# Kernel optimization log

Measured on AMD Instinct MI355X. Metric: run time of the kernel, lower is better.

## Reference

```python
import jax, jax.numpy as jnp
import numpy as np

B, L, DIM, N_STATE, K_CONV = 2, 2048, 1024, 16, 4


def setup_inputs() -> dict:
    key = jax.random.key(0)
    ks = jax.random.split(key, 6)
    sc = lambda k, shape, s: jax.random.normal(k, shape, jnp.float32) * s
    return {
        "x": jax.random.normal(ks[0], (B, L, DIM), jnp.float32),
        "in_proj_w": sc(ks[1], (2 * DIM, DIM), 0.02),
        "conv_w": sc(ks[2], (DIM, 1, K_CONV), 0.1),
        "conv_b": jnp.zeros((DIM,), jnp.float32),
        "x_proj_w": sc(ks[3], (2 * N_STATE + DIM, DIM), 0.02),
        "D_param": jnp.ones((DIM,), jnp.float32),
        "out_proj_w": sc(ks[4], (DIM, DIM), 0.02),
    }


def reference(x, in_proj_w, conv_w, conv_b, x_proj_w, D_param, out_proj_w):
    b, l, d = x.shape
    n = (x_proj_w.shape[0] - d) // 2
    k = conv_w.shape[-1]
    # A buffer: -[1..n] broadcast over channels -> [d, n]
    A = -(jnp.arange(1, n + 1, dtype=x.dtype)[None, :] * jnp.ones((d, 1), x.dtype))

    xz = x @ in_proj_w.T                       # [b, l, 2d]
    x_c, z = xz[..., :d], xz[..., d:]

    # depthwise causal conv (torch pads both sides k-1 then truncates to l == left-pad k-1)
    xc = jnp.transpose(x_c, (0, 2, 1))          # [b, d, l]
    xc = jax.lax.conv_general_dilated(
        xc, conv_w, window_strides=(1,), padding=[(k - 1, 0)],
        dimension_numbers=("NCH", "OIH", "NCH"), feature_group_count=d)
    xc = xc + conv_b[None, :, None]
    xc = jax.nn.silu(jnp.transpose(xc, (0, 2, 1)))  # [b, l, d]

    x_dbl = xc @ x_proj_w.T                    # [b, l, 2n + d]
    B_ssm = x_dbl[..., :n]                     # [b, l, n]
    C_ssm = x_dbl[..., n:2 * n]                # [b, l, n]
    dt = jax.nn.softplus(x_dbl[..., 2 * n:])   # [b, l, d]

    dA = jnp.exp(dt[..., None] * A[None, None])            # [b, l, d, n]
    dBx = (dt[..., None] * B_ssm[:, :, None, :]) * xc[..., None]  # dB * x, [b, l, d, n]

    def step(h, inputs):
        dA_t, dBx_t, C_t = inputs              # [b,d,n], [b,d,n], [b,n]
        h = h * dA_t + dBx_t
        y_t = jnp.einsum("bdn,bn->bd", h, C_t)
        return h, y_t

    h0 = jnp.zeros((b, d, n), x.dtype)
    _, ys = jax.lax.scan(
        step, h0,
        (jnp.moveaxis(dA, 1, 0), jnp.moveaxis(dBx, 1, 0), jnp.moveaxis(C_ssm, 1, 0)))
    y = jnp.moveaxis(ys, 0, 1) + D_param * xc  # [b, l, d]
    y = y * jax.nn.silu(z)
    return y @ out_proj_w.T
```

## Files before the change

kernel.cpp:

```cpp
#include <hip/hip_runtime.h>
#include <cmath>

#define BB   2
#define LL   2048
#define DIMD 1024
#define NS   16
#define KC   4
#define ML   (BB*LL)
#define XZ_N (2*DIMD)
#define XD_N (2*NS + DIMD)
#define LC   16
#define NC   (LL/LC)

typedef __attribute__((ext_vector_type(8))) short bf16x8;
typedef __attribute__((ext_vector_type(4))) float f32x4;

__device__ __forceinline__ unsigned short f2bf(float f) {
    union { float f; unsigned u; } v; v.f = f;
    unsigned r = v.u + 0x7FFF + ((v.u >> 16) & 1);
    return (unsigned short)(r >> 16);
}
__device__ __forceinline__ float bf2f(unsigned short u) {
    union { unsigned u; float f; } v; v.u = (unsigned)u << 16;
    return v.f;
}
__device__ __forceinline__ float silu_f(float a) {
    return a / (1.f + __expf(-a));
}
__device__ __forceinline__ void dt_decay(float raw, float& dt, float& e) {
    const float t = __expf(fminf(raw, 80.f));
    e  = 1.f / (1.f + t);
    dt = (raw > 15.f) ? raw : -__logf(e);
}

__global__ __launch_bounds__(256) void cvt_all(
    const float* __restrict__ s0, unsigned short* __restrict__ d0, int n0,
    const float* __restrict__ s1, unsigned short* __restrict__ d1, int n1,
    const float* __restrict__ s2, unsigned short* __restrict__ d2, int n2,
    const float* __restrict__ s3, unsigned short* __restrict__ d3, int n3)
{
    int i = blockIdx.x * blockDim.x + threadIdx.x;
    const float* src; unsigned short* dst;
    if (i < n0)                { src = s0; dst = d0; }
    else if ((i -= n0) < n1)   { src = s1; dst = d1; }
    else if ((i -= n1) < n2)   { src = s2; dst = d2; }
    else if ((i -= n2) < n3)   { src = s3; dst = d3; }
    else return;
    float4 f = ((const float4*)src)[i];
    ushort4 o;
    o.x = f2bf(f.x); o.y = f2bf(f.y); o.z = f2bf(f.z); o.w = f2bf(f.w);
    ((ushort4*)dst)[i] = o;
}

__global__ __launch_bounds__(256) void gemm_mfma_bt(
    const unsigned short* __restrict__ A,
    const unsigned short* __restrict__ Bw,
    float* __restrict__ C,
    unsigned short* __restrict__ zb,
    int M, int N, int K, int nsplit)
{
    __shared__ short As[2][128 * 64];
    __shared__ short Bs[2][64 * 64];

    const int nwg  = gridDim.x * gridDim.y;
    int wgid = blockIdx.y * gridDim.x + blockIdx.x;
    const int cpx = nwg >> 3;
    wgid = (wgid & 7) * cpx + (wgid >> 3);
    const int bx = wgid % gridDim.x;
    const int by = wgid / gridDim.x;

    const int tid  = threadIdx.x;
    const int lane = tid & 63;
    const int wave = tid >> 6;
    const int bm = by * 128;
    const int bn = bx * 64;
    const int wm = wave * 32;
    const int l15  = lane & 15;
    const int quad = lane >> 4;

    f32x4 acc[2][4];
    #pragma unroll
    for (int i = 0; i < 2; ++i)
        #pragma unroll
        for (int j = 0; j < 4; ++j)
            acc[i][j] = (f32x4){0.f, 0.f, 0.f, 0.f};

    const int NK = K >> 6;

    auto stage = [&](int s, int k0) {
        #pragma unroll
        for (int q = 0; q < 4; ++q) {
            const int ci = q * 256 + tid;
            const int r  = ci >> 3;
            const int cc = (ci & 7) ^ (r & 7);
            short* ldsA = &As[s][0] + (size_t)(q * 256 + (tid & ~63)) * 8;
            const unsigned short* ga = A + (size_t)(bm + r) * K + k0 + cc * 8;
            __builtin_amdgcn_global_load_lds(
                (const __attribute__((address_space(1))) void*)ga,
                (__attribute__((address_space(3))) void*)ldsA, 16, 0, 0);
        }
        #pragma unroll
        for (int q = 0; q < 2; ++q) {
            const int ci = q * 256 + tid;
            const int r  = ci >> 3;
            const int cc = (ci & 7) ^ (r & 7);
            short* ldsB = &Bs[s][0] + (size_t)(q * 256 + (tid & ~63)) * 8;
            int rb = bn + r; if (rb > N - 1) rb = N - 1;
            const unsigned short* gb = Bw + (size_t)rb * K + k0 + cc * 8;
            __builtin_amdgcn_global_load_lds(
                (const __attribute__((address_space(1))) void*)gb,
                (__attribute__((address_space(3))) void*)ldsB, 16, 0, 0);
        }
    };

    stage(0, 0);

    int cur = 0;
    for (int t = 0; t < NK; ++t) {
        if (t + 1 < NK) {
            stage(cur ^ 1, (t + 1) * 64);
            asm volatile("s_waitcnt vmcnt(6)" ::: "memory");
        } else {
            asm volatile("s_waitcnt vmcnt(0)" ::: "memory");
        }
        __builtin_amdgcn_s_barrier();

        const short* Ab = &As[cur][0];
        const short* Bb = &Bs[cur][0];
        #pragma unroll
        for (int kh = 0; kh < 2; ++kh) {
            bf16x8 af[2], bfr[4];
            #pragma unroll
            for (int i = 0; i < 2; ++i) {
                const int row = wm + i * 16 + l15;
                const int pc  = (kh * 4 + quad) ^ (row & 7);
                af[i] = *(const bf16x8*)(Ab + row * 64 + pc * 8);
            }
            #pragma unroll
            for (int j = 0; j < 4; ++j) {
                const int row = j * 16 + l15;
                const int pc  = (kh * 4 + quad) ^ (row & 7);
                bfr[j] = *(const bf16x8*)(Bb + row * 64 + pc * 8);
            }
            #pragma unroll
            for (int i = 0; i < 2; ++i)
                #pragma unroll
                for (int j = 0; j < 4; ++j)
                    acc[i][j] = __builtin_amdgcn_mfma_f32_16x16x32_bf16(
                        af[i], bfr[j], acc[i][j], 0, 0, 0);
        }

        if (t + 1 < NK) __builtin_amdgcn_s_barrier();
        cur ^= 1;
    }

    #pragma unroll
    for (int i = 0; i < 2; ++i) {
        const int rbase = bm + wm + i * 16 + quad * 4;
        #pragma unroll
        for (int j = 0; j < 4; ++j) {
            const int col = bn + j * 16 + l15;
            if (col < nsplit) {
                #pragma unroll
                for (int r = 0; r < 4; ++r)
                    C[(size_t)(rbase + r) * nsplit + col] = acc[i][j][r];
            } else if (col < N) {
                const int zc = col - nsplit;
                #pragma unroll
                for (int r = 0; r < 4; ++r)
                    zb[(size_t)(rbase + r) * DIMD + zc] = f2bf(silu_f(acc[i][j][r]));
            }
        }
    }
}

__global__ __launch_bounds__(256) void conv_silu(const float* __restrict__ xcraw,
                                                 const float* __restrict__ w,
                                                 const float* __restrict__ bias,
                                                 float* __restrict__ xc,
                                                 unsigned short* __restrict__ xcb)
{
    const int i4 = blockIdx.x * blockDim.x + threadIdx.x;
    if (i4 >= ML * DIMD / 4) return;
    const int dq = i4 & (DIMD / 4 - 1);
    const int bl = i4 >> 8;
    const int l  = bl & (LL - 1);

    const float4 wq0 = ((const float4*)w)[dq * 4 + 0];
    const float4 wq1 = ((const float4*)w)[dq * 4 + 1];
    const float4 wq2 = ((const float4*)w)[dq * 4 + 2];
    const float4 wq3 = ((const float4*)w)[dq * 4 + 3];
    const float4 bv  = ((const float4*)bias)[dq];

    const float* p = xcraw + (size_t)bl * DIMD + dq * 4;
    const float4 z4 = make_float4(0.f, 0.f, 0.f, 0.f);
    const float4 x0 = (l >= 3) ? *(const float4*)(p - 3 * DIMD) : z4;
    const float4 x1 = (l >= 2) ? *(const float4*)(p - 2 * DIMD) : z4;
    const float4 x2 = (l >= 1) ? *(const float4*)(p - 1 * DIMD) : z4;
    const float4 x3 = *(const float4*)p;

    float4 a;
    a.x = bv.x + wq0.x*x0.x + wq0.y*x1.x + wq0.z*x2.x + wq0.w*x3.x;
    a.y = bv.y + wq1.x*x0.y + wq1.y*x1.y + wq1.z*x2.y + wq1.w*x3.y;
    a.z = bv.z + wq2.x*x0.z + wq2.y*x1.z + wq2.z*x2.z + wq2.w*x3.z;
    a.w = bv.w + wq3.x*x0.w + wq3.y*x1.w + wq3.z*x2.w + wq3.w*x3.w;

    float4 v;
    v.x = silu_f(a.x); v.y = silu_f(a.y); v.z = silu_f(a.z); v.w = silu_f(a.w);

    ((float4*)xc)[i4] = v;
    ushort4 o;
    o.x = f2bf(v.x); o.y = f2bf(v.y); o.z = f2bf(v.z); o.w = f2bf(v.w);
    ((ushort4*)xcb)[i4] = o;
}

__global__ __launch_bounds__(256) void scan_part1(const float* __restrict__ xdbl,
                                                  const float* __restrict__ xc,
                                                  float* __restrict__ hfin,
                                                  float* __restrict__ Ssum)
{
    __shared__ float Bsh[LC][NS];

    const int tid = threadIdx.x;
    const int idx = blockIdx.x * 256 + tid;
    const int d   = idx & (DIMD - 1);
    const int bc  = idx >> 10;
    const int c   = bc & (NC - 1);
    const int b   = bc >> 7;
    const int l0  = c * LC;

    const float* xdbl_p = xdbl + ((size_t)b * LL + l0) * XD_N;
    const float* xc_p   = xc   + ((size_t)b * LL + l0) * DIMD + d;

    if (tid < LC * NS / 4) {
        const int l = tid >> 2, q = tid & 3;
        ((float4*)&Bsh[l][0])[q] = ((const float4*)(xdbl_p + (size_t)l * XD_N))[q];
    }
    __syncthreads();

    float raw[LC], xcv[LC];
    #pragma unroll
    for (int i = 0; i < LC; ++i) raw[i] = xdbl_p[(size_t)i * XD_N + 2 * NS + d];
    #pragma unroll
    for (int i = 0; i < LC; ++i) xcv[i] = xc_p[(size_t)i * DIMD];

    float e[LC], dx[LC];
    float S = 0.f;
    #pragma unroll
    for (int i = 0; i < LC; ++i) {
        float dt, ev;
        dt_decay(raw[i], dt, ev);
        S += dt;
        e[i]  = ev;
        dx[i] = dt * xcv[i];
    }

    float h[NS];
    #pragma unroll
    for (int n = 0; n < NS; ++n) h[n] = 0.f;

    #pragma unroll
    for (int i = 0; i < LC; ++i) {
        const float4* BC = (const float4*)&Bsh[i][0];
        const float4 B0 = BC[0], B1 = BC[1], B2 = BC[2], B3 = BC[3];
        const float ev = e[i], dxv = dx[i];
        const float e2 = ev * ev, e4 = e2 * e2;
        float p0 = ev, p1 = e2, p2 = e2 * ev, p3 = e4;
        h[0]  = fmaf(h[0],  p0, dxv * B0.x);
        h[1]  = fmaf(h[1],  p1, dxv * B0.y);
        h[2]  = fmaf(h[2],  p2, dxv * B0.z);
        h[3]  = fmaf(h[3],  p3, dxv * B0.w);
        p0 *= e4; p1 *= e4; p2 *= e4; p3 *= e4;
        h[4]  = fmaf(h[4],  p0, dxv * B1.x);
        h[5]  = fmaf(h[5],  p1, dxv * B1.y);
        h[6]  = fmaf(h[6],  p2, dxv * B1.z);
        h[7]  = fmaf(h[7],  p3, dxv * B1.w);
        p0 *= e4; p1 *= e4; p2 *= e4; p3 *= e4;
        h[8]  = fmaf(h[8],  p0, dxv * B2.x);
        h[9]  = fmaf(h[9],  p1, dxv * B2.y);
        h[10] = fmaf(h[10], p2, dxv * B2.z);
        h[11] = fmaf(h[11], p3, dxv * B2.w);
        p0 *= e4; p1 *= e4; p2 *= e4; p3 *= e4;
        h[12] = fmaf(h[12], p0, dxv * B3.x);
        h[13] = fmaf(h[13], p1, dxv * B3.y);
        h[14] = fmaf(h[14], p2, dxv * B3.z);
        h[15] = fmaf(h[15], p3, dxv * B3.w);
    }

    float4* hf = (float4*)(hfin + (size_t)idx * NS);
    #pragma unroll
    for (int n = 0; n < 4; ++n) hf[n] = ((float4*)h)[n];
    Ssum[idx] = S;
}

__global__ __launch_bounds__(64) void scan_combine(float* __restrict__ hfin,
                                                   const float* __restrict__ Ssum)
{
    const int idx = blockIdx.x * blockDim.x + threadIdx.x;
    const int n = idx & (NS - 1);
    const int d = (idx >> 4) & (DIMD - 1);
    const int b = idx >> 14;
    const float np1 = (float)(n + 1);

    float hc = 0.f;
    for (int c0 = 0; c0 < NC; c0 += 8) {
        float Sb[8], hb[8], eb[8];
        #pragma unroll
        for (int j = 0; j < 8; ++j) {
            const size_t base = ((size_t)(b * NC + c0 + j) * DIMD + d);
            Sb[j] = Ssum[base];
            hb[j] = hfin[base * NS + n];
        }
        #pragma unroll
        for (int j = 0; j < 8; ++j) eb[j] = __expf(-Sb[j] * np1);
        #pragma unroll
        for (int j = 0; j < 8; ++j) {
            const size_t o = ((size_t)(b * NC + c0 + j) * DIMD + d) * NS + n;
            hfin[o] = hc;
            hc = fmaf(hc, eb[j], hb[j]);
        }
    }
}

__global__ __launch_bounds__(256) void scan_part2(const float* __restrict__ xdbl,
                                                  const float* __restrict__ xc,
                                                  const unsigned short* __restrict__ zb,
                                                  const float* __restrict__ hfin,
                                                  const float* __restrict__ Dp,
                                                  unsigned short* __restrict__ yout)
{
    __shared__ float BCs[LC][2 * NS];

    const int tid = threadIdx.x;
    const int idx = blockIdx.x * 256 + tid;
    const int d   = idx & (DIMD - 1);
    const int bc  = idx >> 10;
    const int c   = bc & (NC - 1);
    const int b   = bc >> 7;
    const int l0  = c * LC;

    const float* xdbl_p = xdbl + ((size_t)b * LL + l0) * XD_N;
    const float* xc_p   = xc   + ((size_t)b * LL + l0) * DIMD + d;
    const unsigned short* zb_p = zb + ((size_t)b * LL + l0) * DIMD + d;
    unsigned short* y_p = yout + ((size_t)b * LL + l0) * DIMD + d;

    if (tid < LC * 2 * NS / 4) {
        const int l = tid >> 3, q = tid & 7;
        ((float4*)&BCs[l][0])[q] = ((const float4*)(xdbl_p + (size_t)l * XD_N))[q];
    }
    __syncthreads();

    float raw[LC], xcv[LC], zg[LC];
    #pragma unroll
    for (int i = 0; i < LC; ++i) raw[i] = xdbl_p[(size_t)i * XD_N + 2 * NS + d];
    #pragma unroll
    for (int i = 0; i < LC; ++i) xcv[i] = xc_p[(size_t)i * DIMD];
    #pragma unroll
    for (int i = 0; i < LC; ++i) zg[i] = bf2f(zb_p[(size_t)i * DIMD]);

    float e[LC], dx[LC];
    #pragma unroll
    for (int i = 0; i < LC; ++i) {
        float dt, ev;
        dt_decay(raw[i], dt, ev);
        e[i]  = ev;
        dx[i] = dt * xcv[i];
    }

    const float Dv = Dp[d];
    float h[NS];
    {
        const float4* hf = (const float4*)(hfin + (size_t)idx * NS);
        #pragma unroll
        for (int n = 0; n < 4; ++n) ((float4*)h)[n] = hf[n];
    }

    #pragma unroll
    for (int i = 0; i < LC; ++i) {
        const float4* BC = (const float4*)&BCs[i][0];
        const float4 B0 = BC[0], B1 = BC[1], B2 = BC[2], B3 = BC[3];
        const float4 C0 = BC[4], C1 = BC[5], C2 = BC[6], C3 = BC[7];
        const float ev = e[i], dxv = dx[i];
        const float e2 = ev * ev, e4 = e2 * e2;
        float p0 = ev, p1 = e2, p2 = e2 * ev, p3 = e4;
        float y0, y1, y2, y3;
        h[0]  = fmaf(h[0],  p0, dxv * B0.x); y0 = h[0]  * C0.x;
        h[1]  = fmaf(h[1],  p1, dxv * B0.y); y1 = h[1]  * C0.y;
        h[2]  = fmaf(h[2],  p2, dxv * B0.z); y2 = h[2]  * C0.z;
        h[3]  = fmaf(h[3],  p3, dxv * B0.w); y3 = h[3]  * C0.w;
        p0 *= e4; p1 *= e4; p2 *= e4; p3 *= e4;
        h[4]  = fmaf(h[4],  p0, dxv * B1.x); y0 = fmaf(h[4],  C1.x, y0);
        h[5]  = fmaf(h[5],  p1, dxv * B1.y); y1 = fmaf(h[5],  C1.y, y1);
        h[6]  = fmaf(h[6],  p2, dxv * B1.z); y2 = fmaf(h[6],  C1.z, y2);
        h[7]  = fmaf(h[7],  p3, dxv * B1.w); y3 = fmaf(h[7],  C1.w, y3);
        p0 *= e4; p1 *= e4; p2 *= e4; p3 *= e4;
        h[8]  = fmaf(h[8],  p0, dxv * B2.x); y0 = fmaf(h[8],  C2.x, y0);
        h[9]  = fmaf(h[9],  p1, dxv * B2.y); y1 = fmaf(h[9],  C2.y, y1);
        h[10] = fmaf(h[10], p2, dxv * B2.z); y2 = fmaf(h[10], C2.z, y2);
        h[11] = fmaf(h[11], p3, dxv * B2.w); y3 = fmaf(h[11], C2.w, y3);
        p0 *= e4; p1 *= e4; p2 *= e4; p3 *= e4;
        h[12] = fmaf(h[12], p0, dxv * B3.x); y0 = fmaf(h[12], C3.x, y0);
        h[13] = fmaf(h[13], p1, dxv * B3.y); y1 = fmaf(h[13], C3.y, y1);
        h[14] = fmaf(h[14], p2, dxv * B3.z); y2 = fmaf(h[14], C3.z, y2);
        h[15] = fmaf(h[15], p3, dxv * B3.w); y3 = fmaf(h[15], C3.w, y3);

        const float y  = (y0 + y1) + (y2 + y3);
        const float yv = fmaf(Dv, xcv[i], y);
        y_p[(size_t)i * DIMD] = f2bf(yv * zg[i]);
    }
}

extern "C" void kernel_launch(void* const* d_in, const int* in_sizes, int n_in,
                              void* d_out, int out_size, void* d_ws, size_t ws_size,
                              hipStream_t stream)
{
    const float* x          = (const float*)d_in[0];
    const float* in_proj_w  = (const float*)d_in[1];
    const float* conv_w     = (const float*)d_in[2];
    const float* conv_b     = (const float*)d_in[3];
    const float* x_proj_w   = (const float*)d_in[4];
    const float* D_param    = (const float*)d_in[5];
    const float* out_proj_w = (const float*)d_in[6];
    float* out = (float*)d_out;

    float* xcraw = (float*)d_ws;
    float* xc    = xcraw + (size_t)ML * DIMD;
    float* xdbl  = xc    + (size_t)ML * DIMD;
    unsigned short* zb  = (unsigned short*)(xdbl + (size_t)ML * XD_N);
    unsigned short* xb  = zb  + (size_t)ML * DIMD;
    unsigned short* xcb = xb  + (size_t)ML * DIMD;
    unsigned short* wb1 = xcb + (size_t)ML * DIMD;
    unsigned short* wb2 = wb1 + (size_t)XZ_N * DIMD;
    unsigned short* wb3 = wb2 + (size_t)XD_N * DIMD;
    float* hfin = (float*)(wb3 + (size_t)DIMD * DIMD);
    float* Ssum = hfin + (size_t)BB * NC * DIMD * NS;
    unsigned short* yb  = xb;

    const int n0 = ML * DIMD / 4, n1 = XZ_N * DIMD / 4,
              n2 = XD_N * DIMD / 4, n3 = DIMD * DIMD / 4;
    const int ncvt = n0 + n1 + n2 + n3;

    cvt_all<<<(ncvt + 255) / 256, 256, 0, stream>>>(
        x, xb, n0, in_proj_w, wb1, n1, x_proj_w, wb2, n2, out_proj_w, wb3, n3);

    gemm_mfma_bt<<<dim3(XZ_N / 64, ML / 128), 256, 0, stream>>>(
        xb, wb1, xcraw, zb, ML, XZ_N, DIMD, DIMD);

    conv_silu<<<(ML * DIMD / 4) / 256, 256, 0, stream>>>(
        xcraw, conv_w, conv_b, xc, xcb);

    gemm_mfma_bt<<<dim3((XD_N + 63) / 64, ML / 128), 256, 0, stream>>>(
        xcb, wb2, xdbl, nullptr, ML, XD_N, DIMD, XD_N);

    scan_part1<<<(BB * NC * DIMD) / 256, 256, 0, stream>>>(xdbl, xc, hfin, Ssum);
    scan_combine<<<(BB * DIMD * NS) / 64, 64, 0, stream>>>(hfin, Ssum);
    scan_part2<<<(BB * NC * DIMD) / 256, 256, 0, stream>>>(xdbl, xc, zb, hfin,
                                                           D_param, yb);

    gemm_mfma_bt<<<dim3(DIMD / 64, ML / 128), 256, 0, stream>>>(
        yb, wb3, out, nullptr, ML, DIMD, DIMD, DIMD);
}
```

Measured before the change: 214.5 us.

## Parallelize chunk-state combine across chunk groups with two-level scan

The combine kernel previously ran a serial scan over all 128 chunks per (b,d,n) thread with 64-thread blocks. It now splits the chunks into 8 groups, computes each group's affine (decay product, offset) in parallel, combines the group prefixes through shared memory, and then rescans locally. This shortens the serial dependency chain and raises the thread count 8x, at the cost of extra multiplies and a block barrier.

```diff
diff --git a/kernel.cpp b/kernel.cpp
--- a/kernel.cpp
+++ b/kernel.cpp
@@ -293,32 +293,48 @@
     Ssum[idx] = S;
 }
 
-__global__ __launch_bounds__(64) void scan_combine(float* __restrict__ hfin,
-                                                   const float* __restrict__ Ssum)
-{
-    const int idx = blockIdx.x * blockDim.x + threadIdx.x;
-    const int n = idx & (NS - 1);
-    const int d = (idx >> 4) & (DIMD - 1);
-    const int b = idx >> 14;
+#define NGRP 8
+#define CPG  (NC / NGRP)
+__global__ __launch_bounds__(256) void scan_combine(float* __restrict__ hfin,
+                                                    const float* __restrict__ Ssum)
+{
+    __shared__ float Ash[2][NGRP][NS];
+    __shared__ float Bsh2[2][NGRP][NS];
+
+    const int tid = threadIdx.x;
+    const int n   = tid & (NS - 1);
+    const int g   = (tid >> 4) & (NGRP - 1);
+    const int d2  = tid >> 7;
+    const int bd  = blockIdx.x * 2 + d2;
+    const int d   = bd & (DIMD - 1);
+    const int b   = bd >> 10;
     const float np1 = (float)(n + 1);
+    const int c0 = g * CPG;
+
+    float e[CPG], hb[CPG];
+    #pragma unroll
+    for (int j = 0; j < CPG; ++j) {
+        const size_t base = ((size_t)(b * NC + c0 + j) * DIMD + d);
+        const float S = Ssum[base];
+        hb[j] = hfin[base * NS + n];
+        e[j]  = __expf(-S * np1);
+    }
+
+    float A = 1.f, Bv = 0.f;
+    #pragma unroll
+    for (int j = 0; j < CPG; ++j) { Bv = fmaf(Bv, e[j], hb[j]); A *= e[j]; }
+
+    Ash[d2][g][n] = A;  Bsh2[d2][g][n] = Bv;
+    __syncthreads();
 
     float hc = 0.f;
-    for (int c0 = 0; c0 < NC; c0 += 8) {
-        float Sb[8], hb[8], eb[8];
-        #pragma unroll
-        for (int j = 0; j < 8; ++j) {
-            const size_t base = ((size_t)(b * NC + c0 + j) * DIMD + d);
-            Sb[j] = Ssum[base];
-            hb[j] = hfin[base * NS + n];
-        }
-        #pragma unroll
-        for (int j = 0; j < 8; ++j) eb[j] = __expf(-Sb[j] * np1);
-        #pragma unroll
-        for (int j = 0; j < 8; ++j) {
-            const size_t o = ((size_t)(b * NC + c0 + j) * DIMD + d) * NS + n;
-            hfin[o] = hc;
-            hc = fmaf(hc, eb[j], hb[j]);
-        }
+    for (int j = 0; j < g; ++j) hc = fmaf(hc, Ash[d2][j][n], Bsh2[d2][j][n]);
+
+    #pragma unroll
+    for (int j = 0; j < CPG; ++j) {
+        const size_t o = ((size_t)(b * NC + c0 + j) * DIMD + d) * NS + n;
+        hfin[o] = hc;
+        hc = fmaf(hc, e[j], hb[j]);
     }
 }
 
@@ -453,7 +469,7 @@
         xcb, wb2, xdbl, nullptr, ML, XD_N, DIMD, XD_N);
 
     scan_part1<<<(BB * NC * DIMD) / 256, 256, 0, stream>>>(xdbl, xc, hfin, Ssum);
-    scan_combine<<<(BB * DIMD * NS) / 64, 64, 0, stream>>>(hfin, Ssum);
+    scan_combine<<<(BB * DIMD) / 2, 256, 0, stream>>>(hfin, Ssum);
     scan_part2<<<(BB * NC * DIMD) / 256, 256, 0, stream>>>(xdbl, xc, zb, hfin,
                                                            D_param, yb);
 
```

New measurement: 211.8 us. No clear change (-1.3%).
